# Optimization experiments

Measured on AMD Instinct MI355X. Metric: run time of the kernel, lower is better.

Reference implementation:

```python
import jax, jax.numpy as jnp
import numpy as np

# Clause structure: 4 unary clauses and 4 binary (joined-space) clauses,
# each with 3 literals; first literal negated ('n' prefix).
U_IDX = np.array([[0, 1, 2], [3, 4, 5], [6, 7, 8], [9, 10, 11]], dtype=np.int32)
U_SIGNS = np.array([[-1.0, 1.0, 1.0]] * 4, dtype=np.float32)
# Joined matrix columns: [u[i1] (0..15), u[i2] (16..31), binary (32..35)]
B_IDX = np.array([[0, 16, 32], [1, 17, 33], [2, 18, 34], [3, 19, 35]], dtype=np.int32)
B_SIGNS = np.array([[-1.0, 1.0, 1.0]] * 4, dtype=np.float32)

N_NODES, N_UNARY = 50000, 16
N_EDGES, N_BINARY = 1600000, 4
INIT_W = 0.5


def setup_inputs() -> dict:
    key = jax.random.key(0)
    k1, k2, k3, k4 = jax.random.split(key, 4)
    unary = jax.random.normal(k1, (N_NODES, N_UNARY), dtype=jnp.float32)
    binary = jax.random.normal(k2, (N_EDGES, N_BINARY), dtype=jnp.float32)
    edge_index = jax.random.randint(k3, (2, N_EDGES), 0, N_NODES, dtype=jnp.int32)
    wu = jnp.full((4,), INIT_W, dtype=jnp.float32)  # learnable unary clause weights
    wb = jnp.full((4,), INIT_W, dtype=jnp.float32)  # learnable binary clause weights
    return {"unary": unary, "binary": binary, "wu": wu, "wb": wb, "edge_index": edge_index}


def _knowledge_enhancer(x, idx, signs, w):
    """x: [R, P]; idx/signs: [C, L]; w: [C]. Returns summed deltas [R, P]."""
    lit = x[:, idx] * signs                                    # [R, C, L] signed literals
    d = (w[:, None] * jax.nn.softmax(lit, axis=-1)) * signs    # [R, C, L] signed deltas
    return jnp.zeros_like(x).at[:, idx].add(d)                 # scatter-sum over clauses


def reference(unary, binary, wu, wb, edge_index):
    i1, i2 = edge_index[0], edge_index[1]
    P = unary.shape[1]
    # Unary knowledge enhancement
    u = unary + _knowledge_enhancer(unary, U_IDX, U_SIGNS, wu)
    # Join: per-edge [u[i1] | u[i2] | binary]
    joined = jnp.concatenate([u[i1], u[i2], binary], axis=1)   # [E, 2P+B]
    d = _knowledge_enhancer(joined, B_IDX, B_SIGNS, wb)        # [E, 2P+B]
    # GroupBy: scatter node blocks back, keep binary block
    n = unary.shape[0]
    delta_up = (jax.ops.segment_sum(d[:, :P], i1, num_segments=n)
                + jax.ops.segment_sum(d[:, P:2 * P], i2, num_segments=n))
    delta_bp = d[:, 2 * P:]
    # activation = identity (default)
    return u + delta_up, binary + delta_bp
```

## Files before the change

kernel.cpp:

```cpp
#include <hip/hip_runtime.h>
#include <hip/hip_bf16.h>

#define N_NODES 50000
#define N_UNARY 16
#define N_EDGES 1600000
#define N_BINARY 4

typedef float vfloat4 __attribute__((ext_vector_type(4)));

#define FP_SCALE 127.0f
#define FP_INV   (1.0f / 127.0f)

#define BUCKET_SHIFT 11
#define BUCKET_NODES 2048
#define N_BUCKETS 25
#define N_GROUPS 50
#define SEG_CAP 73728
#define N_CHUNKS 10

#define SEG_BYTES  ((size_t)N_GROUPS * SEG_CAP * 8)
#define PART_BYTES ((size_t)N_GROUPS * N_CHUNKS * BUCKET_NODES * 8)
#define WS_NEEDED  (SEG_BYTES + 256 + PART_BYTES)

__device__ inline void enhance_u4(const float x[6], float wu0, float wu1,
                                  float u[4]) {
    float l0 = -x[0], l1 = x[1], l2 = x[2];
    float m  = fmaxf(l0, fmaxf(l1, l2));
    float e0 = __expf(l0 - m), e1 = __expf(l1 - m), e2 = __expf(l2 - m);
    float inv = 1.0f / (e0 + e1 + e2);
    u[0] = x[0] - wu0 * e0 * inv;
    u[1] = x[1] + wu0 * e1 * inv;
    u[2] = x[2] + wu0 * e2 * inv;
    float l3 = -x[3], l4 = x[4], l5 = x[5];
    float m2 = fmaxf(l3, fmaxf(l4, l5));
    float f0 = __expf(l3 - m2), f1 = __expf(l4 - m2), f2 = __expf(l5 - m2);
    float inv2 = 1.0f / (f0 + f1 + f2);
    u[3] = x[3] - wu1 * f0 * inv2;
}

__device__ inline void edge_math(const float* unary, const float* binary,
                                 float wu0, float wu1, const float wc[4],
                                 int i1, int i2, int e,
                                 float s0[4], float s1[4],
                                 float* out_b) {
    const float4* u1p = (const float4*)(unary + (size_t)i1 * N_UNARY);
    const float4* u2p = (const float4*)(unary + (size_t)i2 * N_UNARY);
    float4 x1a = u1p[0], x1b = u1p[1];
    float4 x2a = u2p[0], x2b = u2p[1];
    float xa[6] = {x1a.x, x1a.y, x1a.z, x1a.w, x1b.x, x1b.y};
    float xb[6] = {x2a.x, x2a.y, x2a.z, x2a.w, x2b.x, x2b.y};
    float a[4], b[4];
    enhance_u4(xa, wu0, wu1, a);
    enhance_u4(xb, wu0, wu1, b);

    vfloat4 bn = __builtin_nontemporal_load((const vfloat4*)binary + e);
    float bb[4] = {bn.x, bn.y, bn.z, bn.w};
    float ob[4];
#pragma unroll
    for (int c = 0; c < 4; ++c) {
        float l0 = -a[c], l1 = b[c], l2 = bb[c];
        float m  = fmaxf(l0, fmaxf(l1, l2));
        float e0 = __expf(l0 - m);
        float e1 = __expf(l1 - m);
        float e2 = __expf(l2 - m);
        float inv = 1.0f / (e0 + e1 + e2);
        s0[c] = e0 * inv;
        s1[c] = e1 * inv;
        ob[c] = bb[c] + wc[c] * e2 * inv;
    }
    vfloat4 obv = {ob[0], ob[1], ob[2], ob[3]};
    __builtin_nontemporal_store(obv, (vfloat4*)out_b + e);
}

__device__ inline unsigned long long make_rec(const float s[4], int local_id) {
    unsigned v0 = __float2uint_rn(s[0] * FP_SCALE);
    unsigned v1 = __float2uint_rn(s[1] * FP_SCALE);
    unsigned v2 = __float2uint_rn(s[2] * FP_SCALE);
    unsigned v3 = __float2uint_rn(s[3] * FP_SCALE);
    unsigned pl = v0 | (v1 << 7) | (v2 << 14) | (v3 << 21);
    return (unsigned long long)pl | ((unsigned long long)(unsigned)local_id << 28);
}

__device__ inline unsigned long long pack4_16(const float s[4]) {
    unsigned long long a = __float2uint_rn(s[0] * FP_SCALE);
    unsigned long long b = __float2uint_rn(s[1] * FP_SCALE);
    unsigned long long c = __float2uint_rn(s[2] * FP_SCALE);
    unsigned long long d = __float2uint_rn(s[3] * FP_SCALE);
    return a | (b << 16) | (c << 32) | (d << 48);
}

__global__ void kenn_edge_scatter_kernel(const float* __restrict__ unary,
                                         const float* __restrict__ binary,
                                         const float* __restrict__ wu,
                                         const float* __restrict__ wb,
                                         const int* __restrict__ edge_index,
                                         unsigned long long* __restrict__ segs,
                                         unsigned* __restrict__ tails,
                                         float* __restrict__ out_b) {
    __shared__ unsigned l_cnt[N_GROUPS];
    __shared__ unsigned l_gbase[N_GROUPS];

    int tid = threadIdx.x;
    if (tid < N_GROUPS) l_cnt[tid] = 0;
    __syncthreads();

    int e = blockIdx.x * blockDim.x + tid;
    bool valid = (e < N_EDGES);

    int g1 = 0, g2 = 0;
    unsigned pos1 = 0, pos2 = 0;
    unsigned long long rec1 = 0, rec2 = 0;

    if (valid) {
        int i1 = __builtin_nontemporal_load(edge_index + e);
        int i2 = __builtin_nontemporal_load(edge_index + N_EDGES + e);
        float wu0 = wu[0], wu1 = wu[1];
        float wc[4] = {wb[0], wb[1], wb[2], wb[3]};
        float s0[4], s1[4];
        edge_math(unary, binary, wu0, wu1, wc, i1, i2, e, s0, s1, out_b);
        rec1 = make_rec(s0, i1 & (BUCKET_NODES - 1));
        rec2 = make_rec(s1, i2 & (BUCKET_NODES - 1));
        g1 = i1 >> BUCKET_SHIFT;
        g2 = N_BUCKETS + (i2 >> BUCKET_SHIFT);
        pos1 = atomicAdd(&l_cnt[g1], 1u);
        pos2 = atomicAdd(&l_cnt[g2], 1u);
    }
    __syncthreads();
    if (tid < N_GROUPS) {
        unsigned c = l_cnt[tid];
        l_gbase[tid] = c ? atomicAdd(tails + tid, c) : 0u;
    }
    __syncthreads();

    if (valid) {
        unsigned p1 = l_gbase[g1] + pos1;
        unsigned p2 = l_gbase[g2] + pos2;
        if (p1 < SEG_CAP)
            __builtin_nontemporal_store(rec1, segs + (size_t)g1 * SEG_CAP + p1);
        if (p2 < SEG_CAP)
            __builtin_nontemporal_store(rec2, segs + (size_t)g2 * SEG_CAP + p2);
    }
}

__global__ void kenn_reduce_kernel(const unsigned long long* __restrict__ segs,
                                   const unsigned* __restrict__ tails,
                                   unsigned long long* __restrict__ partials) {
    __shared__ unsigned long long lacc[BUCKET_NODES];
    int chunk = blockIdx.x;
    int g     = blockIdx.y;
    int tid   = threadIdx.x;

    for (int i = tid; i < BUCKET_NODES; i += blockDim.x) lacc[i] = 0ull;
    __syncthreads();

    unsigned cnt = tails[g];
    if (cnt > SEG_CAP) cnt = SEG_CAP;
    unsigned csz   = (cnt + N_CHUNKS - 1) / N_CHUNKS;
    unsigned start = chunk * csz;
    unsigned end   = start + csz;
    if (end > cnt) end = cnt;

    const unsigned long long* seg = segs + (size_t)g * SEG_CAP;
    for (unsigned i = start + tid; i < end; i += blockDim.x) {
        unsigned long long r = seg[i];
        unsigned id = (unsigned)(r >> 28);
        unsigned pl = (unsigned)r & 0x0FFFFFFFu;
        unsigned long long exp =
            (unsigned long long)(pl & 127u) |
            ((unsigned long long)(pl & (127u << 7))  << 9)  |
            ((unsigned long long)(pl & (127u << 14)) << 18) |
            ((unsigned long long)(pl & (127u << 21)) << 27);
        atomicAdd(&lacc[id], exp);
    }
    __syncthreads();

    unsigned long long* dst =
        partials + ((size_t)g * N_CHUNKS + chunk) * BUCKET_NODES;
    for (int i = tid; i < BUCKET_NODES; i += blockDim.x)
        __builtin_nontemporal_store(lacc[i], dst + i);
}

__global__ void kenn_node_final_kernel(const float* __restrict__ unary,
                                       const float* __restrict__ wu,
                                       const float* __restrict__ wb,
                                       const unsigned long long* __restrict__ partials,
                                       const unsigned long long* __restrict__ accN,
                                       const unsigned long long* __restrict__ accP,
                                       int use_partials,
                                       float* __restrict__ out_u) {
    int node = blockIdx.x * blockDim.x + threadIdx.x;
    if (node >= N_NODES) return;

    const float4* up = (const float4*)(unary + (size_t)node * N_UNARY);
    float4 x0 = up[0], x1 = up[1], x2 = up[2], x3 = up[3];
    float x[16] = {x0.x, x0.y, x0.z, x0.w,
                   x1.x, x1.y, x1.z, x1.w,
                   x2.x, x2.y, x2.z, x2.w,
                   x3.x, x3.y, x3.z, x3.w};
    float wuc[4] = {wu[0], wu[1], wu[2], wu[3]};

    float y[16];
#pragma unroll
    for (int i = 0; i < 16; ++i) y[i] = x[i];

#pragma unroll
    for (int c = 0; c < 4; ++c) {
        float l0 = -x[3 * c + 0];
        float l1 =  x[3 * c + 1];
        float l2 =  x[3 * c + 2];
        float m  = fmaxf(l0, fmaxf(l1, l2));
        float e0 = __expf(l0 - m);
        float e1 = __expf(l1 - m);
        float e2 = __expf(l2 - m);
        float inv = 1.0f / (e0 + e1 + e2);
        y[3 * c + 0] -= wuc[c] * e0 * inv;
        y[3 * c + 1] += wuc[c] * e1 * inv;
        y[3 * c + 2] += wuc[c] * e2 * inv;
    }

    unsigned long long pn, pp;
    if (use_partials) {
        int bucket = node >> BUCKET_SHIFT;
        int local  = node & (BUCKET_NODES - 1);
        const unsigned long long* pN =
            partials + ((size_t)bucket * N_CHUNKS) * BUCKET_NODES + local;
        const unsigned long long* pP =
            partials + ((size_t)(N_BUCKETS + bucket) * N_CHUNKS) * BUCKET_NODES + local;
        pn = 0ull; pp = 0ull;
#pragma unroll
        for (int c = 0; c < N_CHUNKS; ++c) {
            pn += pN[(size_t)c * BUCKET_NODES];
            pp += pP[(size_t)c * BUCKET_NODES];
        }
    } else {
        pn = accN[node];
        pp = accP[node];
    }

    float wbc[4] = {wb[0], wb[1], wb[2], wb[3]};
    y[0] += wbc[0] * ((float)(int)((pp      ) & 0xffff) - (float)(int)((pn      ) & 0xffff)) * FP_INV;
    y[1] += wbc[1] * ((float)(int)((pp >> 16) & 0xffff) - (float)(int)((pn >> 16) & 0xffff)) * FP_INV;
    y[2] += wbc[2] * ((float)(int)((pp >> 32) & 0xffff) - (float)(int)((pn >> 32) & 0xffff)) * FP_INV;
    y[3] += wbc[3] * ((float)(int)((pp >> 48) & 0xffff) - (float)(int)((pn >> 48) & 0xffff)) * FP_INV;

    float4* op = (float4*)(out_u + (size_t)node * N_UNARY);
    op[0] = make_float4(y[0],  y[1],  y[2],  y[3]);
    op[1] = make_float4(y[4],  y[5],  y[6],  y[7]);
    op[2] = make_float4(y[8],  y[9],  y[10], y[11]);
    op[3] = make_float4(y[12], y[13], y[14], y[15]);
}

__global__ void kenn_edge_atomic_kernel(const float* __restrict__ unary,
                                        const float* __restrict__ binary,
                                        const float* __restrict__ wu,
                                        const float* __restrict__ wb,
                                        const int* __restrict__ edge_index,
                                        unsigned long long* __restrict__ accN,
                                        unsigned long long* __restrict__ accP,
                                        float* __restrict__ out_b) {
    int e = blockIdx.x * blockDim.x + threadIdx.x;
    if (e >= N_EDGES) return;
    int i1 = __builtin_nontemporal_load(edge_index + e);
    int i2 = __builtin_nontemporal_load(edge_index + N_EDGES + e);
    float wu0 = wu[0], wu1 = wu[1];
    float wc[4] = {wb[0], wb[1], wb[2], wb[3]};
    float s0[4], s1[4];
    edge_math(unary, binary, wu0, wu1, wc, i1, i2, e, s0, s1, out_b);
    atomicAdd(accN + i1, pack4_16(s0));
    atomicAdd(accP + i2, pack4_16(s1));
}

extern "C" void kernel_launch(void* const* d_in, const int* in_sizes, int n_in,
                              void* d_out, int out_size, void* d_ws, size_t ws_size,
                              hipStream_t stream) {
    const float* unary      = (const float*)d_in[0];
    const float* binary     = (const float*)d_in[1];
    const float* wu         = (const float*)d_in[2];
    const float* wb         = (const float*)d_in[3];
    const int*   edge_index = (const int*)d_in[4];

    float* out_u = (float*)d_out;
    float* out_b = (float*)d_out + (size_t)N_NODES * N_UNARY;

    if (ws_size >= WS_NEEDED) {
        unsigned long long* segs = (unsigned long long*)d_ws;
        unsigned* tails = (unsigned*)((char*)d_ws + SEG_BYTES);
        unsigned long long* partials =
            (unsigned long long*)((char*)d_ws + SEG_BYTES + 256);

        (void)hipMemsetAsync(tails, 0, N_GROUPS * sizeof(unsigned), stream);
        {
            dim3 block(1024);
            dim3 grid((N_EDGES + 1023) / 1024);
            kenn_edge_scatter_kernel<<<grid, block, 0, stream>>>(
                unary, binary, wu, wb, edge_index, segs, tails, out_b);
        }
        {
            dim3 grid(N_CHUNKS, N_GROUPS);
            kenn_reduce_kernel<<<grid, dim3(256), 0, stream>>>(
                segs, tails, partials);
        }
        {
            dim3 block(256);
            dim3 grid((N_NODES + 255) / 256);
            kenn_node_final_kernel<<<grid, block, 0, stream>>>(
                unary, wu, wb, partials, nullptr, nullptr, 1, out_u);
        }
    } else {
        unsigned long long* accN = (unsigned long long*)d_ws;
        unsigned long long* accP = accN + N_NODES;
        (void)hipMemsetAsync(accN, 0,
                             (size_t)N_NODES * 2 * sizeof(unsigned long long),
                             stream);
        {
            dim3 block(256);
            dim3 grid((N_EDGES + 255) / 256);
            kenn_edge_atomic_kernel<<<grid, block, 0, stream>>>(
                unary, binary, wu, wb, edge_index, accN, accP, out_b);
        }
        {
            dim3 block(256);
            dim3 grid((N_NODES + 255) / 256);
            kenn_node_final_kernel<<<grid, block, 0, stream>>>(
                unary, wu, wb, nullptr, accN, accP, 0, out_u);
        }
    }
}
```

Baseline: 164.2 us.

## Stage scatter records in LDS sorted by bucket for coalesced segment writes

```diff
diff --git a/kernel.cpp b/kernel.cpp
--- a/kernel.cpp
+++ b/kernel.cpp
@@ -17,6 +17,9 @@
 #define N_GROUPS 50
 #define SEG_CAP 73728
 #define N_CHUNKS 10
+
+#define SCAT_BLOCK 1024
+#define SCAT_RECS (2 * SCAT_BLOCK)
 
 #define SEG_BYTES  ((size_t)N_GROUPS * SEG_CAP * 8)
 #define PART_BYTES ((size_t)N_GROUPS * N_CHUNKS * BUCKET_NODES * 8)
@@ -89,22 +92,26 @@
     return a | (b << 16) | (c << 32) | (d << 48);
 }
 
-__global__ void kenn_edge_scatter_kernel(const float* __restrict__ unary,
-                                         const float* __restrict__ binary,
-                                         const float* __restrict__ wu,
-                                         const float* __restrict__ wb,
-                                         const int* __restrict__ edge_index,
-                                         unsigned long long* __restrict__ segs,
-                                         unsigned* __restrict__ tails,
-                                         float* __restrict__ out_b) {
+__global__ void __launch_bounds__(SCAT_BLOCK)
+kenn_edge_scatter_kernel(const float* __restrict__ unary,
+                         const float* __restrict__ binary,
+                         const float* __restrict__ wu,
+                         const float* __restrict__ wb,
+                         const int* __restrict__ edge_index,
+                         unsigned long long* __restrict__ segs,
+                         unsigned* __restrict__ tails,
+                         float* __restrict__ out_b) {
     __shared__ unsigned l_cnt[N_GROUPS];
+    __shared__ unsigned l_pref[N_GROUPS + 1];
     __shared__ unsigned l_gbase[N_GROUPS];
+    __shared__ unsigned long long staged[SCAT_RECS];
+    __shared__ unsigned char staged_g[SCAT_RECS];
 
     int tid = threadIdx.x;
     if (tid < N_GROUPS) l_cnt[tid] = 0;
     __syncthreads();
 
-    int e = blockIdx.x * blockDim.x + tid;
+    int e = blockIdx.x * SCAT_BLOCK + tid;
     bool valid = (e < N_EDGES);
 
     int g1 = 0, g2 = 0;
@@ -126,25 +133,41 @@
         pos2 = atomicAdd(&l_cnt[g2], 1u);
     }
     __syncthreads();
-    if (tid < N_GROUPS) {
-        unsigned c = l_cnt[tid];
-        l_gbase[tid] = c ? atomicAdd(tails + tid, c) : 0u;
+
+    if (tid == 0) {
+        unsigned run = 0;
+#pragma unroll
+        for (int g = 0; g < N_GROUPS; ++g) { l_pref[g] = run; run += l_cnt[g]; }
+        l_pref[N_GROUPS] = run;
+    } else if (tid >= 64 && tid < 64 + N_GROUPS) {
+        int g = tid - 64;
+        unsigned c = l_cnt[g];
+        l_gbase[g] = c ? atomicAdd(tails + g, c) : 0u;
     }
     __syncthreads();
 
     if (valid) {
-        unsigned p1 = l_gbase[g1] + pos1;
-        unsigned p2 = l_gbase[g2] + pos2;
-        if (p1 < SEG_CAP)
-            __builtin_nontemporal_store(rec1, segs + (size_t)g1 * SEG_CAP + p1);
-        if (p2 < SEG_CAP)
-            __builtin_nontemporal_store(rec2, segs + (size_t)g2 * SEG_CAP + p2);
-    }
-}
-
-__global__ void kenn_reduce_kernel(const unsigned long long* __restrict__ segs,
-                                   const unsigned* __restrict__ tails,
-                                   unsigned long long* __restrict__ partials) {
+        unsigned s1p = l_pref[g1] + pos1;
+        unsigned s2p = l_pref[g2] + pos2;
+        staged[s1p] = rec1;  staged_g[s1p] = (unsigned char)g1;
+        staged[s2p] = rec2;  staged_g[s2p] = (unsigned char)g2;
+    }
+    __syncthreads();
+
+    unsigned total = l_pref[N_GROUPS];
+    for (unsigned i = tid; i < total; i += SCAT_BLOCK) {
+        unsigned g = staged_g[i];
+        unsigned long long rec = staged[i];
+        unsigned p = l_gbase[g] + (i - l_pref[g]);
+        if (p < SEG_CAP)
+            __builtin_nontemporal_store(rec, segs + (size_t)g * SEG_CAP + p);
+    }
+}
+
+__global__ void __launch_bounds__(512)
+kenn_reduce_kernel(const unsigned long long* __restrict__ segs,
+                   const unsigned* __restrict__ tails,
+                   unsigned long long* __restrict__ partials) {
     __shared__ unsigned long long lacc[BUCKET_NODES];
     int chunk = blockIdx.x;
     int g     = blockIdx.y;
@@ -163,7 +186,7 @@
     const unsigned long long* seg = segs + (size_t)g * SEG_CAP;
     for (unsigned i = start + tid; i < end; i += blockDim.x) {
         unsigned long long r = seg[i];
-        unsigned id = (unsigned)(r >> 28);
+        unsigned id = (unsigned)(r >> 28) & (BUCKET_NODES - 1);
         unsigned pl = (unsigned)r & 0x0FFFFFFFu;
         unsigned long long exp =
             (unsigned long long)(pl & 127u) |
@@ -290,14 +313,13 @@
 
         (void)hipMemsetAsync(tails, 0, N_GROUPS * sizeof(unsigned), stream);
         {
-            dim3 block(1024);
-            dim3 grid((N_EDGES + 1023) / 1024);
-            kenn_edge_scatter_kernel<<<grid, block, 0, stream>>>(
+            dim3 grid((N_EDGES + SCAT_BLOCK - 1) / SCAT_BLOCK);
+            kenn_edge_scatter_kernel<<<grid, dim3(SCAT_BLOCK), 0, stream>>>(
                 unary, binary, wu, wb, edge_index, segs, tails, out_b);
         }
         {
             dim3 grid(N_CHUNKS, N_GROUPS);
-            kenn_reduce_kernel<<<grid, dim3(256), 0, stream>>>(
+            kenn_reduce_kernel<<<grid, dim3(512), 0, stream>>>(
                 segs, tails, partials);
         }
         {
```

After: 150.9 us. 1.09x faster.
